# Performance work log

Hardware: AMD Instinct MI355X
Metric: run time of the kernel (lower is better)

Reference implementation:

```python
import jax, jax.numpy as jnp
import numpy as np


def setup_inputs() -> dict:
    key0 = jax.random.key(0)
    kq, kk, kv = jax.random.split(key0, 3)
    B, H, L, S, D = 2, 8, 2048, 2048, 64
    query = jax.random.normal(kq, (B, H, L, D), dtype=jnp.float32)
    key = jax.random.normal(kk, (B, H, S, D), dtype=jnp.float32)
    value = jax.random.normal(kv, (B, H, S, D), dtype=jnp.float32)
    return {"query": query, "key": key, "value": value}


def reference(query, key, value):
    # Original computes matmul(q[b,h,l,1,d,1], k[b,h,1,s,1,d]) -> [B,H,L,S,D,D]
    # outer products, divides by sqrt(query.shape[-1]) AFTER unsqueeze (==1, no-op),
    # then sums dims (4,5). That is algebraically exactly rowsum(q)*rowsum(k).
    qsum = query.sum(axis=-1)                       # [B,H,L]
    ksum = key.sum(axis=-1)                         # [B,H,S]
    score = qsum[..., :, None] * ksum[..., None, :]  # [B,H,L,S]
    attn = jax.nn.softmax(score, axis=-1)            # softmax over S
    out = jnp.einsum('bhls,bhsd->bhld', attn, value)  # [B,H,L,D]
    return out
```

## Files before the change

kernel.cpp:

```cpp
#include <hip/hip_runtime.h>
#include <hip/hip_bf16.h>

#define BH 16
#define L 2048
#define S 2048
#define DD 64
#define BM 64
#define BK 64
#define LDSPAD 8
#define LDW (BK + LDSPAD)

typedef __attribute__((ext_vector_type(4))) float f32x4;
typedef __bf16 bf16x8 __attribute__((ext_vector_type(8)));

union FragU {
  bf16x8 f;
  __hip_bfloat162 h2[4];
};

__device__ inline __hip_bfloat162 exp2pack(float al2, float nsl2, float k0,
                                           float k1, float& d) {
  float e0 = __builtin_amdgcn_exp2f(fmaf(al2, k0, nsl2));
  float e1 = __builtin_amdgcn_exp2f(fmaf(al2, k1, nsl2));
  d += e0 + e1;
  return __float22bfloat162_rn(make_float2(e0, e1));
}

__global__ __launch_bounds__(256) void prep_kernel(
    const float* __restrict__ k, const float* __restrict__ v,
    float* __restrict__ ks, __hip_bfloat16* __restrict__ vt) {
  __shared__ __hip_bfloat16 tile[DD][LDW];
  int t = threadIdx.x;
  if (blockIdx.x < 2048) {
    int g = blockIdx.x * 256 + t;
    int row = g >> 4;
    int l16 = g & 15;
    float4 x = reinterpret_cast<const float4*>(k + (size_t)row * DD)[l16];
    float s = x.x + x.y + x.z + x.w;
    s += __shfl_xor(s, 1);
    s += __shfl_xor(s, 2);
    s += __shfl_xor(s, 4);
    s += __shfl_xor(s, 8);
    if (l16 == 0) ks[row] = s;
  } else {
    int bid = blockIdx.x - 2048;
    int bh = (bid & 7) * 2 + ((bid >> 3) & 1);
    int st = bid >> 4;
    int s0 = st * 64;
    int srow = t >> 4;
    int d4 = (t & 15) * 4;
#pragma unroll
    for (int kk = 0; kk < 4; ++kk) {
      int s = srow + kk * 16;
      float4 val = *reinterpret_cast<const float4*>(
          v + ((size_t)(bh * S + s0 + s)) * DD + d4);
      tile[d4 + 0][s] = __float2bfloat16(val.x);
      tile[d4 + 1][s] = __float2bfloat16(val.y);
      tile[d4 + 2][s] = __float2bfloat16(val.z);
      tile[d4 + 3][s] = __float2bfloat16(val.w);
    }
    __syncthreads();
    __hip_bfloat16* tb = vt + ((size_t)(bh * 32 + st)) * (DD * 64);
    int dd = t >> 3;
    int j = t & 7;
#pragma unroll
    for (int kk = 0; kk < 2; ++kk) {
      int d = dd + kk * 32;
      uint4 val = *reinterpret_cast<const uint4*>(&tile[d][j * 8]);
      *reinterpret_cast<uint4*>(tb + d * 64 + j * 8) = val;
    }
  }
}

__global__ __launch_bounds__(256) void attn_kernel(
    const float* __restrict__ q, const __hip_bfloat16* __restrict__ vt,
    const float* __restrict__ ks, float* __restrict__ out) {
  int bx = blockIdx.x;
  int bh = (bx & 7) * 2 + ((bx >> 3) & 1);
  int l0 = (bx >> 4) * BM;

  __shared__ __hip_bfloat16 ldsVT[2][DD][LDW];
  __shared__ float a_row[BM];
  __shared__ float red[16];

  int t = threadIdx.x;
  int lane = t & 63;
  int w = t >> 6;
  int m = lane & 15;
  int qd = lane >> 4;

  const __hip_bfloat16* vtb = vt + ((size_t)bh * 32) * (DD * 64);
  const float* ksb = ks + (size_t)bh * S;

  uint4 v0 = *reinterpret_cast<const uint4*>(vtb + t * 8);
  uint4 v1 = *reinterpret_cast<const uint4*>(vtb + 2048 + t * 8);
  float4 kA0 = *reinterpret_cast<const float4*>(ksb + qd * 8);
  float4 kA1 = *reinterpret_cast<const float4*>(ksb + qd * 8 + 4);
  float4 kB0 = *reinterpret_cast<const float4*>(ksb + 32 + qd * 8);
  float4 kB1 = *reinterpret_cast<const float4*>(ksb + 32 + qd * 8 + 4);

  {
    int r = t >> 2;
    int p = t & 3;
    const float* qp = q + ((size_t)(bh * L + l0 + r)) * DD + p * 16;
    float4 x0 = reinterpret_cast<const float4*>(qp)[0];
    float4 x1 = reinterpret_cast<const float4*>(qp)[1];
    float4 x2 = reinterpret_cast<const float4*>(qp)[2];
    float4 x3 = reinterpret_cast<const float4*>(qp)[3];
    float s = (x0.x + x0.y + x0.z + x0.w) + (x1.x + x1.y + x1.z + x1.w) +
              (x2.x + x2.y + x2.z + x2.w) + (x3.x + x3.y + x3.z + x3.w);
    s += __shfl_xor(s, 1);
    s += __shfl_xor(s, 2);
    if (p == 0) a_row[r] = s;
  }

  {
    const float* kp = ksb + t * 8;
    float4 y0 = reinterpret_cast<const float4*>(kp)[0];
    float4 y1 = reinterpret_cast<const float4*>(kp)[1];
    float mx = fmaxf(fmaxf(fmaxf(y0.x, y0.y), fmaxf(y0.z, y0.w)),
                     fmaxf(fmaxf(y1.x, y1.y), fmaxf(y1.z, y1.w)));
    float mn = fminf(fminf(fminf(y0.x, y0.y), fminf(y0.z, y0.w)),
                     fminf(fminf(y1.x, y1.y), fminf(y1.z, y1.w)));
#pragma unroll
    for (int off = 1; off < 64; off <<= 1) {
      mx = fmaxf(mx, __shfl_xor(mx, off));
      mn = fminf(mn, __shfl_xor(mn, off));
    }
    if (lane == 0) {
      red[w] = mx;
      red[8 + w] = mn;
    }
  }
  __syncthreads();

  float kmax = fmaxf(fmaxf(red[0], red[1]), fmaxf(red[2], red[3]));
  float kmin = fminf(fminf(red[8], red[9]), fminf(red[10], red[11]));
  float ar = a_row[w * 16 + m];
  float sel = (ar > 0.f) ? kmax : kmin;
  const float LOG2E = 1.44269504088896f;
  float al2 = ar * LOG2E;
  float nsl2 = -al2 * sel;

  float dsum = 0.f;
  f32x4 acc[4];
#pragma unroll
  for (int c = 0; c < 4; ++c) acc[c] = (f32x4){0.f, 0.f, 0.f, 0.f};

  for (int it = 0; it < 32; ++it) {
    int bufi = it & 1;
    *reinterpret_cast<uint4*>(&ldsVT[bufi][t >> 3][(t & 7) * 8]) = v0;
    *reinterpret_cast<uint4*>(&ldsVT[bufi][32 + (t >> 3)][(t & 7) * 8]) = v1;
    __syncthreads();

    int itn = (it < 31) ? it + 1 : 31;
    const __hip_bfloat16* tn = vtb + (size_t)itn * (DD * 64);
    v0 = *reinterpret_cast<const uint4*>(tn + t * 8);
    v1 = *reinterpret_cast<const uint4*>(tn + 2048 + t * 8);
    int s0n = itn * BK;

    FragU f0, f1;
    f0.h2[0] = exp2pack(al2, nsl2, kA0.x, kA0.y, dsum);
    f0.h2[1] = exp2pack(al2, nsl2, kA0.z, kA0.w, dsum);
    f0.h2[2] = exp2pack(al2, nsl2, kA1.x, kA1.y, dsum);
    f0.h2[3] = exp2pack(al2, nsl2, kA1.z, kA1.w, dsum);
    f1.h2[0] = exp2pack(al2, nsl2, kB0.x, kB0.y, dsum);
    f1.h2[1] = exp2pack(al2, nsl2, kB0.z, kB0.w, dsum);
    f1.h2[2] = exp2pack(al2, nsl2, kB1.x, kB1.y, dsum);
    f1.h2[3] = exp2pack(al2, nsl2, kB1.z, kB1.w, dsum);

    kA0 = *reinterpret_cast<const float4*>(ksb + s0n + qd * 8);
    kA1 = *reinterpret_cast<const float4*>(ksb + s0n + qd * 8 + 4);
    kB0 = *reinterpret_cast<const float4*>(ksb + s0n + 32 + qd * 8);
    kB1 = *reinterpret_cast<const float4*>(ksb + s0n + 32 + qd * 8 + 4);

#pragma unroll
    for (int c = 0; c < 4; ++c) {
      uint4 bu0 =
          *reinterpret_cast<const uint4*>(&ldsVT[bufi][c * 16 + m][qd * 8]);
      acc[c] = __builtin_amdgcn_mfma_f32_16x16x32_bf16(
          f0.f, __builtin_bit_cast(bf16x8, bu0), acc[c], 0, 0, 0);
      uint4 bu1 = *reinterpret_cast<const uint4*>(
          &ldsVT[bufi][c * 16 + m][32 + qd * 8]);
      acc[c] = __builtin_amdgcn_mfma_f32_16x16x32_bf16(
          f1.f, __builtin_bit_cast(bf16x8, bu1), acc[c], 0, 0, 0);
    }
  }

  float dt = dsum;
  dt += __shfl_xor(dt, 16);
  dt += __shfl_xor(dt, 32);
  float inv[4];
#pragma unroll
  for (int i = 0; i < 4; ++i) inv[i] = 1.0f / __shfl(dt, qd * 4 + i);

  float* ob = out + ((size_t)(bh * L + l0 + w * 16)) * DD;
#pragma unroll
  for (int c = 0; c < 4; ++c) {
#pragma unroll
    for (int i = 0; i < 4; ++i) {
      ob[(size_t)(qd * 4 + i) * DD + c * 16 + m] = acc[c][i] * inv[i];
    }
  }
}

extern "C" void kernel_launch(void* const* d_in, const int* in_sizes, int n_in,
                              void* d_out, int out_size, void* d_ws,
                              size_t ws_size, hipStream_t stream) {
  const float* q = (const float*)d_in[0];
  const float* k = (const float*)d_in[1];
  const float* v = (const float*)d_in[2];
  float* out = (float*)d_out;
  float* ws = (float*)d_ws;

  float* ks = ws;
  __hip_bfloat16* vt = (__hip_bfloat16*)(ws + BH * S);

  prep_kernel<<<2048 + 512, 256, 0, stream>>>(k, v, ks, vt);
  attn_kernel<<<(L / BM) * BH, 256, 0, stream>>>(q, vt, ks, out);
}
```

Before: 100.3 us.

## Halve row tile and split key dimension across waves with LDS reduction

The row tile shrinks from 64 to 32, doubling the number of blocks. Each pair of waves now splits the 64-wide key chunk in half, so every wave does half the exp2 work and half the MFMAs per iteration. Partial numerators and denominators are reduced through LDS, then written out as coalesced float4 stores. In exchange, V tile loads per output row double, and the epilogue gains extra LDS traffic and a barrier.

```diff
diff --git a/kernel.cpp b/kernel.cpp
--- a/kernel.cpp
+++ b/kernel.cpp
@@ -5,10 +5,11 @@
 #define L 2048
 #define S 2048
 #define DD 64
-#define BM 64
+#define BM 32
 #define BK 64
 #define LDSPAD 8
 #define LDW (BK + LDSPAD)
+#define NPITCH 68
 
 typedef __attribute__((ext_vector_type(4))) float f32x4;
 typedef __bf16 bf16x8 __attribute__((ext_vector_type(8)));
@@ -80,6 +81,8 @@
   int l0 = (bx >> 4) * BM;
 
   __shared__ __hip_bfloat16 ldsVT[2][DD][LDW];
+  __shared__ float numLDS[4][16][NPITCH];
+  __shared__ float dLDS[4][16];
   __shared__ float a_row[BM];
   __shared__ float red[16];
 
@@ -88,29 +91,27 @@
   int w = t >> 6;
   int m = lane & 15;
   int qd = lane >> 4;
+  int rt = (w & 1) * 16;
+  int kh = (w >> 1) * 32;
 
   const __hip_bfloat16* vtb = vt + ((size_t)bh * 32) * (DD * 64);
   const float* ksb = ks + (size_t)bh * S;
 
   uint4 v0 = *reinterpret_cast<const uint4*>(vtb + t * 8);
   uint4 v1 = *reinterpret_cast<const uint4*>(vtb + 2048 + t * 8);
-  float4 kA0 = *reinterpret_cast<const float4*>(ksb + qd * 8);
-  float4 kA1 = *reinterpret_cast<const float4*>(ksb + qd * 8 + 4);
-  float4 kB0 = *reinterpret_cast<const float4*>(ksb + 32 + qd * 8);
-  float4 kB1 = *reinterpret_cast<const float4*>(ksb + 32 + qd * 8 + 4);
+  float4 kv0 = *reinterpret_cast<const float4*>(ksb + kh + qd * 8);
+  float4 kv1 = *reinterpret_cast<const float4*>(ksb + kh + qd * 8 + 4);
 
   {
-    int r = t >> 2;
-    int p = t & 3;
-    const float* qp = q + ((size_t)(bh * L + l0 + r)) * DD + p * 16;
+    int r = t >> 3;
+    int p = t & 7;
+    const float* qp = q + ((size_t)(bh * L + l0 + r)) * DD + p * 8;
     float4 x0 = reinterpret_cast<const float4*>(qp)[0];
     float4 x1 = reinterpret_cast<const float4*>(qp)[1];
-    float4 x2 = reinterpret_cast<const float4*>(qp)[2];
-    float4 x3 = reinterpret_cast<const float4*>(qp)[3];
-    float s = (x0.x + x0.y + x0.z + x0.w) + (x1.x + x1.y + x1.z + x1.w) +
-              (x2.x + x2.y + x2.z + x2.w) + (x3.x + x3.y + x3.z + x3.w);
+    float s = (x0.x + x0.y + x0.z + x0.w) + (x1.x + x1.y + x1.z + x1.w);
     s += __shfl_xor(s, 1);
     s += __shfl_xor(s, 2);
+    s += __shfl_xor(s, 4);
     if (p == 0) a_row[r] = s;
   }
 
@@ -136,7 +137,7 @@
 
   float kmax = fmaxf(fmaxf(red[0], red[1]), fmaxf(red[2], red[3]));
   float kmin = fminf(fminf(red[8], red[9]), fminf(red[10], red[11]));
-  float ar = a_row[w * 16 + m];
+  float ar = a_row[rt + m];
   float sel = (ar > 0.f) ? kmax : kmin;
   const float LOG2E = 1.44269504088896f;
   float al2 = ar * LOG2E;
@@ -159,48 +160,52 @@
     v1 = *reinterpret_cast<const uint4*>(tn + 2048 + t * 8);
     int s0n = itn * BK;
 
-    FragU f0, f1;
-    f0.h2[0] = exp2pack(al2, nsl2, kA0.x, kA0.y, dsum);
-    f0.h2[1] = exp2pack(al2, nsl2, kA0.z, kA0.w, dsum);
-    f0.h2[2] = exp2pack(al2, nsl2, kA1.x, kA1.y, dsum);
-    f0.h2[3] = exp2pack(al2, nsl2, kA1.z, kA1.w, dsum);
-    f1.h2[0] = exp2pack(al2, nsl2, kB0.x, kB0.y, dsum);
-    f1.h2[1] = exp2pack(al2, nsl2, kB0.z, kB0.w, dsum);
-    f1.h2[2] = exp2pack(al2, nsl2, kB1.x, kB1.y, dsum);
-    f1.h2[3] = exp2pack(al2, nsl2, kB1.z, kB1.w, dsum);
-
-    kA0 = *reinterpret_cast<const float4*>(ksb + s0n + qd * 8);
-    kA1 = *reinterpret_cast<const float4*>(ksb + s0n + qd * 8 + 4);
-    kB0 = *reinterpret_cast<const float4*>(ksb + s0n + 32 + qd * 8);
-    kB1 = *reinterpret_cast<const float4*>(ksb + s0n + 32 + qd * 8 + 4);
+    FragU f0;
+    f0.h2[0] = exp2pack(al2, nsl2, kv0.x, kv0.y, dsum);
+    f0.h2[1] = exp2pack(al2, nsl2, kv0.z, kv0.w, dsum);
+    f0.h2[2] = exp2pack(al2, nsl2, kv1.x, kv1.y, dsum);
+    f0.h2[3] = exp2pack(al2, nsl2, kv1.z, kv1.w, dsum);
+
+    kv0 = *reinterpret_cast<const float4*>(ksb + s0n + kh + qd * 8);
+    kv1 = *reinterpret_cast<const float4*>(ksb + s0n + kh + qd * 8 + 4);
 
 #pragma unroll
     for (int c = 0; c < 4; ++c) {
-      uint4 bu0 =
-          *reinterpret_cast<const uint4*>(&ldsVT[bufi][c * 16 + m][qd * 8]);
+      uint4 bu =
+          *reinterpret_cast<const uint4*>(&ldsVT[bufi][c * 16 + m][kh + qd * 8]);
       acc[c] = __builtin_amdgcn_mfma_f32_16x16x32_bf16(
-          f0.f, __builtin_bit_cast(bf16x8, bu0), acc[c], 0, 0, 0);
-      uint4 bu1 = *reinterpret_cast<const uint4*>(
-          &ldsVT[bufi][c * 16 + m][32 + qd * 8]);
-      acc[c] = __builtin_amdgcn_mfma_f32_16x16x32_bf16(
-          f1.f, __builtin_bit_cast(bf16x8, bu1), acc[c], 0, 0, 0);
+          f0.f, __builtin_bit_cast(bf16x8, bu), acc[c], 0, 0, 0);
     }
   }
 
   float dt = dsum;
   dt += __shfl_xor(dt, 16);
   dt += __shfl_xor(dt, 32);
-  float inv[4];
-#pragma unroll
-  for (int i = 0; i < 4; ++i) inv[i] = 1.0f / __shfl(dt, qd * 4 + i);
-
-  float* ob = out + ((size_t)(bh * L + l0 + w * 16)) * DD;
-#pragma unroll
-  for (int c = 0; c < 4; ++c) {
-#pragma unroll
-    for (int i = 0; i < 4; ++i) {
-      ob[(size_t)(qd * 4 + i) * DD + c * 16 + m] = acc[c][i] * inv[i];
-    }
+  if (qd == 0) dLDS[w][m] = dt;
+#pragma unroll
+  for (int c = 0; c < 4; ++c)
+#pragma unroll
+    for (int i = 0; i < 4; ++i)
+      numLDS[w][qd * 4 + i][c * 16 + m] = acc[c][i];
+  __syncthreads();
+
+  {
+    int r = t >> 3;
+    int cg = (t & 7) * 8;
+    int wlo = (r >> 4) & 1;
+    int rr = r & 15;
+    float4 n0 = *reinterpret_cast<const float4*>(&numLDS[wlo][rr][cg]);
+    float4 n1 = *reinterpret_cast<const float4*>(&numLDS[wlo][rr][cg + 4]);
+    float4 p0 = *reinterpret_cast<const float4*>(&numLDS[wlo + 2][rr][cg]);
+    float4 p1 = *reinterpret_cast<const float4*>(&numLDS[wlo + 2][rr][cg + 4]);
+    n0.x += p0.x; n0.y += p0.y; n0.z += p0.z; n0.w += p0.w;
+    n1.x += p1.x; n1.y += p1.y; n1.z += p1.z; n1.w += p1.w;
+    float inv = 1.0f / (dLDS[wlo][rr] + dLDS[wlo + 2][rr]);
+    n0.x *= inv; n0.y *= inv; n0.z *= inv; n0.w *= inv;
+    n1.x *= inv; n1.y *= inv; n1.z *= inv; n1.w *= inv;
+    float* ob = out + ((size_t)(bh * L + l0 + r)) * DD + cg;
+    reinterpret_cast<float4*>(ob)[0] = n0;
+    reinterpret_cast<float4*>(ob)[1] = n1;
   }
 }
 
```

Result: no change. 101.0 us (+0.7%).

## Split attention waves across rows and key halves with LDS cross-wave reduction

Applied to the files above, without the earlier changes.

Each wave now computes two 16-row tiles over half of each 128-wide key chunk, so every LDS B-fragment load feeds two MFMAs and the number of loop iterations and barriers is halved. Partial numerators and denominators from the two key-half waves are combined through LDS before normalisation and written with coalesced float4 stores. The cost is extra LDS for the partial sums, an additional barrier, more accumulator registers, and double the exp work per wave per iteration.

```diff
diff --git a/kernel.cpp b/kernel.cpp
--- a/kernel.cpp
+++ b/kernel.cpp
@@ -6,9 +6,11 @@
 #define S 2048
 #define DD 64
 #define BM 64
-#define BK 64
+#define BK 128
 #define LDSPAD 8
-#define LDW (BK + LDSPAD)
+#define LDW2 (BK + LDSPAD)
+#define LDWP (DD + LDSPAD)
+#define NPITCH 68
 
 typedef __attribute__((ext_vector_type(4))) float f32x4;
 typedef __bf16 bf16x8 __attribute__((ext_vector_type(8)));
@@ -29,7 +31,7 @@
 __global__ __launch_bounds__(256) void prep_kernel(
     const float* __restrict__ k, const float* __restrict__ v,
     float* __restrict__ ks, __hip_bfloat16* __restrict__ vt) {
-  __shared__ __hip_bfloat16 tile[DD][LDW];
+  __shared__ __hip_bfloat16 tile[DD][LDWP];
   int t = threadIdx.x;
   if (blockIdx.x < 2048) {
     int g = blockIdx.x * 256 + t;
@@ -79,7 +81,9 @@
   int bh = (bx & 7) * 2 + ((bx >> 3) & 1);
   int l0 = (bx >> 4) * BM;
 
-  __shared__ __hip_bfloat16 ldsVT[2][DD][LDW];
+  __shared__ __hip_bfloat16 ldsVT[2][DD][LDW2];
+  __shared__ float numLDS[4][32][NPITCH];
+  __shared__ float dLDS[4][32];
   __shared__ float a_row[BM];
   __shared__ float red[16];
 
@@ -88,16 +92,21 @@
   int w = t >> 6;
   int m = lane & 15;
   int qd = lane >> 4;
+  int wr = w & 1;
+  int wk = w >> 1;
+  int kh = wk * 32;
 
   const __hip_bfloat16* vtb = vt + ((size_t)bh * 32) * (DD * 64);
   const float* ksb = ks + (size_t)bh * S;
 
   uint4 v0 = *reinterpret_cast<const uint4*>(vtb + t * 8);
   uint4 v1 = *reinterpret_cast<const uint4*>(vtb + 2048 + t * 8);
-  float4 kA0 = *reinterpret_cast<const float4*>(ksb + qd * 8);
-  float4 kA1 = *reinterpret_cast<const float4*>(ksb + qd * 8 + 4);
-  float4 kB0 = *reinterpret_cast<const float4*>(ksb + 32 + qd * 8);
-  float4 kB1 = *reinterpret_cast<const float4*>(ksb + 32 + qd * 8 + 4);
+  uint4 v2 = *reinterpret_cast<const uint4*>(vtb + 4096 + t * 8);
+  uint4 v3 = *reinterpret_cast<const uint4*>(vtb + 6144 + t * 8);
+  float4 kv0 = *reinterpret_cast<const float4*>(ksb + kh + qd * 8);
+  float4 kv1 = *reinterpret_cast<const float4*>(ksb + kh + qd * 8 + 4);
+  float4 kv2 = *reinterpret_cast<const float4*>(ksb + 64 + kh + qd * 8);
+  float4 kv3 = *reinterpret_cast<const float4*>(ksb + 64 + kh + qd * 8 + 4);
 
   {
     int r = t >> 2;
@@ -136,70 +145,120 @@
 
   float kmax = fmaxf(fmaxf(red[0], red[1]), fmaxf(red[2], red[3]));
   float kmin = fminf(fminf(red[8], red[9]), fminf(red[10], red[11]));
-  float ar = a_row[w * 16 + m];
-  float sel = (ar > 0.f) ? kmax : kmin;
   const float LOG2E = 1.44269504088896f;
-  float al2 = ar * LOG2E;
-  float nsl2 = -al2 * sel;
-
-  float dsum = 0.f;
-  f32x4 acc[4];
-#pragma unroll
-  for (int c = 0; c < 4; ++c) acc[c] = (f32x4){0.f, 0.f, 0.f, 0.f};
-
-  for (int it = 0; it < 32; ++it) {
+  float ar0 = a_row[wr * 32 + m];
+  float ar1 = a_row[wr * 32 + 16 + m];
+  float al20 = ar0 * LOG2E, al21 = ar1 * LOG2E;
+  float nsl20 = -al20 * ((ar0 > 0.f) ? kmax : kmin);
+  float nsl21 = -al21 * ((ar1 > 0.f) ? kmax : kmin);
+
+  float ds0 = 0.f, ds1 = 0.f;
+  f32x4 acc[2][4];
+#pragma unroll
+  for (int a = 0; a < 2; ++a)
+#pragma unroll
+    for (int c = 0; c < 4; ++c) acc[a][c] = (f32x4){0.f, 0.f, 0.f, 0.f};
+
+  for (int it = 0; it < S / BK; ++it) {
     int bufi = it & 1;
-    *reinterpret_cast<uint4*>(&ldsVT[bufi][t >> 3][(t & 7) * 8]) = v0;
-    *reinterpret_cast<uint4*>(&ldsVT[bufi][32 + (t >> 3)][(t & 7) * 8]) = v1;
+    {
+      int d = t >> 3;
+      int s8 = (t & 7) * 8;
+      *reinterpret_cast<uint4*>(&ldsVT[bufi][d][s8]) = v0;
+      *reinterpret_cast<uint4*>(&ldsVT[bufi][32 + d][s8]) = v1;
+      *reinterpret_cast<uint4*>(&ldsVT[bufi][d][64 + s8]) = v2;
+      *reinterpret_cast<uint4*>(&ldsVT[bufi][32 + d][64 + s8]) = v3;
+    }
     __syncthreads();
 
-    int itn = (it < 31) ? it + 1 : 31;
-    const __hip_bfloat16* tn = vtb + (size_t)itn * (DD * 64);
+    int itn = (it < S / BK - 1) ? it + 1 : it;
+    const __hip_bfloat16* tn = vtb + (size_t)itn * (2 * DD * 64);
     v0 = *reinterpret_cast<const uint4*>(tn + t * 8);
     v1 = *reinterpret_cast<const uint4*>(tn + 2048 + t * 8);
+    v2 = *reinterpret_cast<const uint4*>(tn + 4096 + t * 8);
+    v3 = *reinterpret_cast<const uint4*>(tn + 6144 + t * 8);
     int s0n = itn * BK;
 
     FragU f0, f1;
-    f0.h2[0] = exp2pack(al2, nsl2, kA0.x, kA0.y, dsum);
-    f0.h2[1] = exp2pack(al2, nsl2, kA0.z, kA0.w, dsum);
-    f0.h2[2] = exp2pack(al2, nsl2, kA1.x, kA1.y, dsum);
-    f0.h2[3] = exp2pack(al2, nsl2, kA1.z, kA1.w, dsum);
-    f1.h2[0] = exp2pack(al2, nsl2, kB0.x, kB0.y, dsum);
-    f1.h2[1] = exp2pack(al2, nsl2, kB0.z, kB0.w, dsum);
-    f1.h2[2] = exp2pack(al2, nsl2, kB1.x, kB1.y, dsum);
-    f1.h2[3] = exp2pack(al2, nsl2, kB1.z, kB1.w, dsum);
-
-    kA0 = *reinterpret_cast<const float4*>(ksb + s0n + qd * 8);
-    kA1 = *reinterpret_cast<const float4*>(ksb + s0n + qd * 8 + 4);
-    kB0 = *reinterpret_cast<const float4*>(ksb + s0n + 32 + qd * 8);
-    kB1 = *reinterpret_cast<const float4*>(ksb + s0n + 32 + qd * 8 + 4);
-
+    f0.h2[0] = exp2pack(al20, nsl20, kv0.x, kv0.y, ds0);
+    f0.h2[1] = exp2pack(al20, nsl20, kv0.z, kv0.w, ds0);
+    f0.h2[2] = exp2pack(al20, nsl20, kv1.x, kv1.y, ds0);
+    f0.h2[3] = exp2pack(al20, nsl20, kv1.z, kv1.w, ds0);
+    f1.h2[0] = exp2pack(al21, nsl21, kv0.x, kv0.y, ds1);
+    f1.h2[1] = exp2pack(al21, nsl21, kv0.z, kv0.w, ds1);
+    f1.h2[2] = exp2pack(al21, nsl21, kv1.x, kv1.y, ds1);
+    f1.h2[3] = exp2pack(al21, nsl21, kv1.z, kv1.w, ds1);
 #pragma unroll
     for (int c = 0; c < 4; ++c) {
-      uint4 bu0 =
-          *reinterpret_cast<const uint4*>(&ldsVT[bufi][c * 16 + m][qd * 8]);
-      acc[c] = __builtin_amdgcn_mfma_f32_16x16x32_bf16(
-          f0.f, __builtin_bit_cast(bf16x8, bu0), acc[c], 0, 0, 0);
-      uint4 bu1 = *reinterpret_cast<const uint4*>(
-          &ldsVT[bufi][c * 16 + m][32 + qd * 8]);
-      acc[c] = __builtin_amdgcn_mfma_f32_16x16x32_bf16(
-          f1.f, __builtin_bit_cast(bf16x8, bu1), acc[c], 0, 0, 0);
-    }
-  }
-
-  float dt = dsum;
-  dt += __shfl_xor(dt, 16);
-  dt += __shfl_xor(dt, 32);
-  float inv[4];
-#pragma unroll
-  for (int i = 0; i < 4; ++i) inv[i] = 1.0f / __shfl(dt, qd * 4 + i);
-
-  float* ob = out + ((size_t)(bh * L + l0 + w * 16)) * DD;
-#pragma unroll
-  for (int c = 0; c < 4; ++c) {
-#pragma unroll
-    for (int i = 0; i < 4; ++i) {
-      ob[(size_t)(qd * 4 + i) * DD + c * 16 + m] = acc[c][i] * inv[i];
+      uint4 bu =
+          *reinterpret_cast<const uint4*>(&ldsVT[bufi][c * 16 + m][kh + qd * 8]);
+      bf16x8 bf = __builtin_bit_cast(bf16x8, bu);
+      acc[0][c] = __builtin_amdgcn_mfma_f32_16x16x32_bf16(f0.f, bf, acc[0][c],
+                                                          0, 0, 0);
+      acc[1][c] = __builtin_amdgcn_mfma_f32_16x16x32_bf16(f1.f, bf, acc[1][c],
+                                                          0, 0, 0);
+    }
+
+    f0.h2[0] = exp2pack(al20, nsl20, kv2.x, kv2.y, ds0);
+    f0.h2[1] = exp2pack(al20, nsl20, kv2.z, kv2.w, ds0);
+    f0.h2[2] = exp2pack(al20, nsl20, kv3.x, kv3.y, ds0);
+    f0.h2[3] = exp2pack(al20, nsl20, kv3.z, kv3.w, ds0);
+    f1.h2[0] = exp2pack(al21, nsl21, kv2.x, kv2.y, ds1);
+    f1.h2[1] = exp2pack(al21, nsl21, kv2.z, kv2.w, ds1);
+    f1.h2[2] = exp2pack(al21, nsl21, kv3.x, kv3.y, ds1);
+    f1.h2[3] = exp2pack(al21, nsl21, kv3.z, kv3.w, ds1);
+
+    kv0 = *reinterpret_cast<const float4*>(ksb + s0n + kh + qd * 8);
+    kv1 = *reinterpret_cast<const float4*>(ksb + s0n + kh + qd * 8 + 4);
+    kv2 = *reinterpret_cast<const float4*>(ksb + s0n + 64 + kh + qd * 8);
+    kv3 = *reinterpret_cast<const float4*>(ksb + s0n + 64 + kh + qd * 8 + 4);
+
+#pragma unroll
+    for (int c = 0; c < 4; ++c) {
+      uint4 bu = *reinterpret_cast<const uint4*>(
+          &ldsVT[bufi][c * 16 + m][64 + kh + qd * 8]);
+      bf16x8 bf = __builtin_bit_cast(bf16x8, bu);
+      acc[0][c] = __builtin_amdgcn_mfma_f32_16x16x32_bf16(f0.f, bf, acc[0][c],
+                                                          0, 0, 0);
+      acc[1][c] = __builtin_amdgcn_mfma_f32_16x16x32_bf16(f1.f, bf, acc[1][c],
+                                                          0, 0, 0);
+    }
+  }
+
+  ds0 += __shfl_xor(ds0, 16);
+  ds0 += __shfl_xor(ds0, 32);
+  ds1 += __shfl_xor(ds1, 16);
+  ds1 += __shfl_xor(ds1, 32);
+  if (qd == 0) {
+    dLDS[w][m] = ds0;
+    dLDS[w][16 + m] = ds1;
+  }
+#pragma unroll
+  for (int a = 0; a < 2; ++a)
+#pragma unroll
+    for (int c = 0; c < 4; ++c)
+#pragma unroll
+      for (int i = 0; i < 4; ++i)
+        numLDS[w][a * 16 + qd * 4 + i][c * 16 + m] = acc[a][c][i];
+  __syncthreads();
+
+  {
+    int r = t >> 2;
+    int cg = (t & 3) * 16;
+    int lr = r & 31;
+    int wlo = r >> 5;
+    float inv = 1.0f / (dLDS[wlo][lr] + dLDS[wlo + 2][lr]);
+    float* ob = out + ((size_t)(bh * L + l0 + r)) * DD + cg;
+#pragma unroll
+    for (int u = 0; u < 4; ++u) {
+      float4 n = *reinterpret_cast<const float4*>(&numLDS[wlo][lr][cg + u * 4]);
+      float4 p =
+          *reinterpret_cast<const float4*>(&numLDS[wlo + 2][lr][cg + u * 4]);
+      n.x = (n.x + p.x) * inv;
+      n.y = (n.y + p.y) * inv;
+      n.z = (n.z + p.z) * inv;
+      n.w = (n.w + p.w) * inv;
+      reinterpret_cast<float4*>(ob)[u] = n;
     }
   }
 }
```

New measurement: 98.09 us. 1.02x faster.
